# Kernel tuning notes

Hardware: AMD Instinct MI355X
Metric: run time of the kernel (lower is better)

## Reference

```python
import jax, jax.numpy as jnp
import numpy as np


def _rel_pos_log(ws):
    coords = np.stack(np.meshgrid(np.arange(ws), np.arange(ws), indexing='ij'))  # [2,ws,ws]
    cf = coords.reshape(2, -1)
    rel = (cf[:, :, None] - cf[:, None, :]).transpose(1, 2, 0).astype(np.float32)  # [N,N,2]
    return np.sign(rel) * np.log1p(np.abs(rel))


def _conv1x1(x, w, b):
    return jnp.einsum('bchw,oc->bohw', x, w) + b[None, :, None, None]


def _conv3x3_reflect(x, w, b):
    xp = jnp.pad(x, ((0, 0), (0, 0), (1, 1), (1, 1)), mode='reflect')
    y = jax.lax.conv_general_dilated(xp, w, (1, 1), 'VALID',
                                     dimension_numbers=('NCHW', 'OIHW', 'NCHW'))
    return y + b[None, :, None, None]


def setup_inputs() -> dict:
    key = jax.random.key(0)
    ks = jax.random.split(key, 8)
    dim, nh = 96, 6
    s = 0.02
    return {
        'X': jax.random.normal(ks[0], (4, dim, 256, 256), jnp.float32),
        'V_w': jax.random.normal(ks[1], (dim, dim), jnp.float32) * s,
        'V_b': jnp.zeros((dim,), jnp.float32),
        'QK_w': jax.random.normal(ks[2], (2 * dim, dim), jnp.float32) * s,
        'QK_b': jnp.zeros((2 * dim,), jnp.float32),
        'meta_w1': jax.random.normal(ks[3], (2, 256), jnp.float32) * 0.1,
        'meta_b1': jnp.zeros((256,), jnp.float32),
        'meta_w2': jax.random.normal(ks[4], (256, nh), jnp.float32) * 0.1,
        'meta_b2': jnp.zeros((nh,), jnp.float32),
        'conv1_w': jax.random.normal(ks[5], (dim, dim, 3, 3), jnp.float32) * s,
        'conv1_b': jnp.zeros((dim,), jnp.float32),
        'conv2_w': jax.random.normal(ks[6], (dim, dim, 3, 3), jnp.float32) * s,
        'conv2_b': jnp.zeros((dim,), jnp.float32),
        'proj_w': jax.random.normal(ks[7], (dim, dim), jnp.float32) * s,
        'proj_b': jnp.zeros((dim,), jnp.float32),
        'window_size': 8,
        'num_heads': 6,
    }


def reference(X, V_w, V_b, QK_w, QK_b, meta_w1, meta_b1, meta_w2, meta_b2,
              conv1_w, conv1_b, conv2_w, conv2_b, proj_w, proj_b,
              window_size, num_heads):
    B, C, H, W = X.shape
    ws = int(window_size)
    nh = int(num_heads)
    hd = C // nh
    scale = hd ** (-0.5)

    V = _conv1x1(X, V_w, V_b)                     # [B,C,H,W]
    QK = _conv1x1(X, QK_w, QK_b)                  # [B,2C,H,W]
    QKV = jnp.concatenate([QK, V], axis=1)        # [B,3C,H,W]

    # window partition (shift_size=0, H,W divisible by ws -> no padding)
    x = QKV.transpose(0, 2, 3, 1)                 # [B,H,W,3C]
    x = x.reshape(B, H // ws, ws, W // ws, ws, 3 * C)
    x = x.transpose(0, 1, 3, 2, 4, 5).reshape(-1, ws * ws, 3 * C)  # [nW,N,3C]

    qkv = x.reshape(-1, ws * ws, 3, nh, hd).transpose(2, 0, 3, 1, 4)
    q, k, v = qkv[0] * scale, qkv[1], qkv[2]      # [nW,nh,N,hd]
    attn = jnp.einsum('bhnd,bhmd->bhnm', q, k)    # [nW,nh,N,N]

    rp = jnp.asarray(_rel_pos_log(ws))            # [N,N,2]
    bias = jax.nn.relu(rp @ meta_w1 + meta_b1) @ meta_w2 + meta_b2  # [N,N,nh]
    attn = attn + bias.transpose(2, 0, 1)[None]
    attn = jax.nn.softmax(attn, axis=-1)

    o = jnp.einsum('bhnm,bhmd->bhnd', attn, v)    # [nW,nh,N,hd]
    o = o.transpose(0, 2, 1, 3).reshape(-1, ws * ws, C)

    # window reverse
    o = o.reshape(B, H // ws, W // ws, ws, ws, C)
    o = o.transpose(0, 1, 3, 2, 4, 5).reshape(B, H, W, C)
    attn_out = o.transpose(0, 3, 1, 2)            # [B,C,H,W]

    conv_out = _conv3x3_reflect(jax.nn.relu(_conv3x3_reflect(V, conv1_w, conv1_b)),
                                conv2_w, conv2_b)
    out = _conv1x1(conv_out + attn_out, proj_w, proj_b)
    return out
```

## Files before the change

### kernel.cpp

```cpp
#include <hip/hip_runtime.h>
#include <cmath>

typedef short  short8 __attribute__((ext_vector_type(8)));
typedef float  f32x4  __attribute__((ext_vector_type(4)));
typedef unsigned short us8 __attribute__((ext_vector_type(8)));
typedef unsigned short us4 __attribute__((ext_vector_type(4)));

constexpr int kHW = 65536;
constexpr int kP  = 262144;

__device__ __forceinline__ unsigned short f2bf(float x) {
  unsigned u = __builtin_bit_cast(unsigned, x);
  u += 0x7fffu + ((u >> 16) & 1u);
  return (unsigned short)(u >> 16);
}
__device__ __forceinline__ float bf2f(unsigned short h) {
  unsigned u = ((unsigned)h) << 16;
  return __builtin_bit_cast(float, u);
}
__device__ __forceinline__ void split2(float v, unsigned short& h, unsigned short& l) {
  unsigned short hh = f2bf(v);
  h = hh;
  l = f2bf(v - bf2f(hh));
}

__global__ void bias_kernel(const float* __restrict__ w1, const float* __restrict__ b1,
                            const float* __restrict__ w2, const float* __restrict__ b2,
                            float* __restrict__ bias_tab) {
  int i = blockIdx.x;
  int j = threadIdx.x;
  float dy = (float)((i >> 3) - (j >> 3));
  float dx = (float)((i & 7) - (j & 7));
  float r0 = copysignf(log1pf(fabsf(dy)), dy);
  float r1 = copysignf(log1pf(fabsf(dx)), dx);
  float acc[6];
#pragma unroll
  for (int h = 0; h < 6; ++h) acc[h] = b2[h];
  for (int t = 0; t < 256; ++t) {
    float hv = fmaf(r0, w1[t], fmaf(r1, w1[256 + t], b1[t]));
    hv = fmaxf(hv, 0.f);
#pragma unroll
    for (int h = 0; h < 6; ++h) acc[h] = fmaf(hv, w2[t * 6 + h], acc[h]);
  }
#pragma unroll
  for (int h = 0; h < 6; ++h) bias_tab[h * 4096 + i * 64 + j] = acc[h];
}

__global__ void prep_weights(const float* __restrict__ qk_w, const float* __restrict__ v_w,
                             const float* __restrict__ c1w, const float* __restrict__ c2w,
                             const float* __restrict__ pjw,
                             unsigned short* __restrict__ Wqh, unsigned short* __restrict__ Wql,
                             unsigned short* __restrict__ W1h,
                             unsigned short* __restrict__ W2h,
                             unsigned short* __restrict__ Wph, unsigned short* __restrict__ Wpl) {
  int i = blockIdx.x * 256 + threadIdx.x;
  if (i < 27648) {
    float v = (i < 18432) ? qk_w[i] : v_w[i - 18432];
    split2(v, Wqh[i], Wql[i]);
  }
  if (i < 82944) {
    int dlt = i / 9216;
    int oc  = (i / 96) % 96;
    int ic  = i % 96;
    int src = (oc * 96 + ic) * 9 + dlt;
    W1h[i] = f2bf(c1w[src]);
    W2h[i] = f2bf(c2w[src]);
  }
  if (i < 9216) split2(pjw[i], Wph[i], Wpl[i]);
}

__global__ __launch_bounds__(256) void split_x(const float* __restrict__ X,
                                               unsigned short* __restrict__ Xh) {
  __shared__ float tile[96][65];
  int t = threadIdx.x;
  size_t p0 = (size_t)blockIdx.x * 64;
  int b = (int)(p0 >> 16), pix = (int)(p0 & 65535);
  const float* xb = X + (size_t)b * 96 * kHW + pix;
#pragma unroll
  for (int i = 0; i < 24; ++i) {
    int ic = (t >> 6) + i * 4;
    tile[ic][t & 63] = xb[(size_t)ic * kHW + (t & 63)];
  }
  __syncthreads();
  int px = t >> 2;
  size_t outbase = (p0 + px) * 96;
#pragma unroll
  for (int cc = 0; cc < 3; ++cc) {
    int c = (t & 3) + cc * 4;
    us8 h8;
#pragma unroll
    for (int j = 0; j < 8; ++j) h8[j] = f2bf(tile[c * 8 + j][px]);
    *(us8*)(Xh + outbase + c * 8) = h8;
  }
}

__global__ __launch_bounds__(256, 2) void qkv_gemm(
    const unsigned short* __restrict__ Wqh, const unsigned short* __restrict__ Wql,
    const unsigned short* __restrict__ Xh,
    const float* __restrict__ qk_b, const float* __restrict__ v_b,
    unsigned short* __restrict__ Qp, unsigned short* __restrict__ Kp,
    unsigned short* __restrict__ Vp) {
  int t = threadIdx.x, wv = t >> 6, lane = t & 63;
  size_t px0 = (size_t)blockIdx.x * 256 + wv * 64;
  int col = lane & 15, g = lane >> 4;

  const char* bH = (const char*)Xh + ((px0 + col) * 96 + g * 8) * 2;
  short8 Bh[3][4];
#pragma unroll
  for (int ks = 0; ks < 3; ++ks)
#pragma unroll
    for (int nf = 0; nf < 4; ++nf)
      Bh[ks][nf] = *(const short8*)(bH + (size_t)(nf * 16 * 96 + ks * 32) * 2);

#pragma unroll 1
  for (int z = 0; z < 3; ++z) {
    f32x4 acc[6][4];
#pragma unroll
    for (int m = 0; m < 6; ++m)
#pragma unroll
      for (int n = 0; n < 4; ++n) acc[m][n] = (f32x4)0.f;
    const char* aH = (const char*)(Wqh + z * 9216) + (size_t)(col * 96 + g * 8) * 2;
    const char* aL = (const char*)(Wql + z * 9216) + (size_t)(col * 96 + g * 8) * 2;
#pragma unroll
    for (int ks = 0; ks < 3; ++ks) {
      short8 Ah[6], Al[6];
#pragma unroll
      for (int mf = 0; mf < 6; ++mf) {
        Ah[mf] = *(const short8*)(aH + (size_t)(mf * 16 * 96 + ks * 32) * 2);
        Al[mf] = *(const short8*)(aL + (size_t)(mf * 16 * 96 + ks * 32) * 2);
      }
#pragma unroll
      for (int mf = 0; mf < 6; ++mf)
#pragma unroll
        for (int nf = 0; nf < 4; ++nf) {
          acc[mf][nf] = __builtin_amdgcn_mfma_f32_16x16x32_bf16(Ah[mf], Bh[ks][nf], acc[mf][nf], 0, 0, 0);
          acc[mf][nf] = __builtin_amdgcn_mfma_f32_16x16x32_bf16(Al[mf], Bh[ks][nf], acc[mf][nf], 0, 0, 0);
        }
    }
    const float* bias = (z == 0) ? qk_b : (z == 1 ? qk_b + 96 : v_b);
    float scale = (z == 0) ? 0.25f : 1.f;
    unsigned short* dst = (z == 0) ? Qp : (z == 1 ? Kp : Vp);
#pragma unroll
    for (int mf = 0; mf < 6; ++mf) {
      int oc0 = mf * 16 + g * 4;
      int c8 = mf * 2 + (g >> 1);
      f32x4 bv;
#pragma unroll
      for (int r = 0; r < 4; ++r) bv[r] = bias[oc0 + r];
#pragma unroll
      for (int nf = 0; nf < 4; ++nf) {
        size_t p = px0 + nf * 16 + col;
        f32x4 v = (acc[mf][nf] + bv) * scale;
        us4 o;
#pragma unroll
        for (int r = 0; r < 4; ++r) o[r] = f2bf(v[r]);
        *(us4*)(dst + ((size_t)c8 * kP + p) * 8 + (g & 1) * 4) = o;
      }
    }
  }
}

__global__ __launch_bounds__(256) void attn_mfma(
    const unsigned short* __restrict__ Qp, const unsigned short* __restrict__ Kp,
    const unsigned short* __restrict__ Vp, const float* __restrict__ bias_tab,
    unsigned short* __restrict__ out) {
  __shared__ unsigned short PT[4][64 * 72];
  __shared__ unsigned short VT[4][16 * 72];
  __shared__ float rls[4][64];

  int t = threadIdx.x;
  int wv = t >> 6, lane = t & 63;
  int l15 = lane & 15, g = lane >> 4;
  int h = blockIdx.y;
  int wid = blockIdx.x * 4 + wv;
  int b = wid >> 10, wy = (wid >> 5) & 31, wx = wid & 31;
  size_t p0 = ((size_t)b << 16) + (size_t)wy * 8 * 256 + (size_t)wx * 8;
  const float* bt = bias_tab + h * 4096;

  f32x4 acc[4][4];
#pragma unroll
  for (int kf = 0; kf < 4; ++kf)
#pragma unroll
    for (int qf = 0; qf < 4; ++qf)
      acc[kf][qf] = *(const f32x4*)(bt + (qf * 16 + l15) * 64 + kf * 16 + g * 4);

  short8 Af[4], Bf[4];
#pragma unroll
  for (int f = 0; f < 4; ++f) {
    int kk = f * 16 + l15;
    size_t pk = p0 + (size_t)(kk >> 3) * 256 + (kk & 7);
    if (g < 2) {
      size_t pl = (size_t)(2 * h + g) * kP;
      Af[f] = *(const short8*)(Kp + (pl + pk) * 8);
      Bf[f] = *(const short8*)(Qp + (pl + pk) * 8);
    } else {
      Af[f] = (short8)0;
      Bf[f] = (short8)0;
    }
  }

  {
    size_t pv = p0 + (size_t)(lane >> 3) * 256 + (lane & 7);
    us8 v0 = *(const us8*)(Vp + ((size_t)(2 * h) * kP + pv) * 8);
    us8 v1 = *(const us8*)(Vp + ((size_t)(2 * h + 1) * kP + pv) * 8);
    unsigned short* vt = VT[wv];
#pragma unroll
    for (int d = 0; d < 8; ++d) {
      vt[d * 72 + lane]       = v0[d];
      vt[(d + 8) * 72 + lane] = v1[d];
    }
  }

#pragma unroll
  for (int kf = 0; kf < 4; ++kf)
#pragma unroll
    for (int qf = 0; qf < 4; ++qf)
      acc[kf][qf] = __builtin_amdgcn_mfma_f32_16x16x32_bf16(Af[kf], Bf[qf], acc[kf][qf], 0, 0, 0);

#pragma unroll
  for (int qf = 0; qf < 4; ++qf) {
    float m = acc[0][qf][0];
#pragma unroll
    for (int kf = 0; kf < 4; ++kf)
#pragma unroll
      for (int r = 0; r < 4; ++r) m = fmaxf(m, acc[kf][qf][r]);
    m = fmaxf(m, __shfl_xor(m, 16));
    m = fmaxf(m, __shfl_xor(m, 32));
    float sum = 0.f;
#pragma unroll
    for (int kf = 0; kf < 4; ++kf)
#pragma unroll
      for (int r = 0; r < 4; ++r) {
        float pe = __expf(acc[kf][qf][r] - m);
        acc[kf][qf][r] = pe;
        sum += pe;
      }
    sum += __shfl_xor(sum, 16);
    sum += __shfl_xor(sum, 32);
    if (g == 0) rls[wv][qf * 16 + l15] = 1.f / sum;
  }

  unsigned short* pt = PT[wv];
#pragma unroll
  for (int qf = 0; qf < 4; ++qf)
#pragma unroll
    for (int kf = 0; kf < 4; ++kf) {
      us4 pb;
#pragma unroll
      for (int r = 0; r < 4; ++r) pb[r] = f2bf(acc[kf][qf][r]);
      *(us4*)&pt[(qf * 16 + l15) * 72 + kf * 16 + g * 4] = pb;
    }

  short8 Pa[4][2], Vb[2];
#pragma unroll
  for (int qf = 0; qf < 4; ++qf)
#pragma unroll
    for (int kc = 0; kc < 2; ++kc)
      Pa[qf][kc] = *(const short8*)&pt[(qf * 16 + l15) * 72 + kc * 32 + g * 8];
#pragma unroll
  for (int kc = 0; kc < 2; ++kc)
    Vb[kc] = *(const short8*)&VT[wv][l15 * 72 + kc * 32 + g * 8];
  f32x4 o[4];
#pragma unroll
  for (int qf = 0; qf < 4; ++qf) {
    o[qf] = (f32x4)0.f;
#pragma unroll
    for (int kc = 0; kc < 2; ++kc)
      o[qf] = __builtin_amdgcn_mfma_f32_16x16x32_bf16(Pa[qf][kc], Vb[kc], o[qf], 0, 0, 0);
  }

#pragma unroll
  for (int qf = 0; qf < 4; ++qf) {
    f32x4 rv = *(const f32x4*)&rls[wv][qf * 16 + g * 4];
#pragma unroll
    for (int r = 0; r < 4; ++r)
      pt[(qf * 16 + g * 4 + r) * 72 + l15] = f2bf(o[qf][r] * rv[r]);
  }
  {
    int q = lane;
    us8 o0 = *(const us8*)&pt[q * 72];
    us8 o1 = *(const us8*)&pt[q * 72 + 8];
    size_t pq = p0 + (size_t)(q >> 3) * 256 + (q & 7);
    *(us8*)(out + ((size_t)(2 * h) * kP + pq) * 8)     = o0;
    *(us8*)(out + ((size_t)(2 * h + 1) * kP + pq) * 8) = o1;
  }
}

template <int MODE>
__global__ __launch_bounds__(256, 4) void conv_direct(
    const unsigned short* __restrict__ Wh,
    const unsigned short* __restrict__ B_, const float* __restrict__ bias,
    const unsigned short* __restrict__ attn, unsigned short* __restrict__ O_) {
  int t = threadIdx.x, wv = t >> 6, lane = t & 63;
  int col = lane & 15, g = lane >> 4;
  int och = wv >> 1, xq = wv & 1;
  int bid = blockIdx.x;
  int g8 = (bid & 7) * 256 + (bid >> 3);
  int xh = g8 & 1;
  int ry = g8 >> 1;
  int b = ry >> 8, y = ry & 255;
  int x0 = xh * 128 + xq * 64;

  int xc[4][3];
#pragma unroll
  for (int nf = 0; nf < 4; ++nf)
#pragma unroll
    for (int dx = 0; dx < 3; ++dx) {
      int xx = x0 + nf * 16 + col + dx - 1;
      xc[nf][dx] = xx < 0 ? 1 : (xx > 255 ? 254 : xx);
    }

  f32x4 acc[3][4];
#pragma unroll
  for (int m = 0; m < 3; ++m)
#pragma unroll
    for (int n = 0; n < 4; ++n) acc[m][n] = (f32x4)0.f;

  size_t bb = (size_t)b * kHW;
#pragma unroll
  for (int dy = 0; dy < 3; ++dy) {
    int yy = y + dy - 1;
    yy = yy < 0 ? 1 : (yy > 255 ? 254 : yy);
    size_t rowp = bb + (size_t)yy * 256;
#pragma unroll
    for (int dx = 0; dx < 3; ++dx) {
      const char* ah = (const char*)Wh +
          ((size_t)(dy * 3 + dx) * 9216 + och * 4608 + col * 96 + g * 8) * 2;
#pragma unroll
      for (int ks = 0; ks < 3; ++ks) {
        short8 Ah[3], Bf[4];
#pragma unroll
        for (int mf = 0; mf < 3; ++mf)
          Ah[mf] = *(const short8*)(ah + (size_t)(mf * 16 * 96 + ks * 32) * 2);
        size_t plane = (size_t)(ks * 4 + g) * kP;
#pragma unroll
        for (int nf = 0; nf < 4; ++nf)
          Bf[nf] = *(const short8*)(B_ + (plane + rowp + xc[nf][dx]) * 8);
#pragma unroll
        for (int mf = 0; mf < 3; ++mf)
#pragma unroll
          for (int nf = 0; nf < 4; ++nf)
            acc[mf][nf] = __builtin_amdgcn_mfma_f32_16x16x32_bf16(Ah[mf], Bf[nf], acc[mf][nf], 0, 0, 0);
      }
    }
  }

  size_t prow = bb + (size_t)y * 256;
#pragma unroll
  for (int mf = 0; mf < 3; ++mf) {
    int oc0 = och * 48 + mf * 16 + g * 4;
    int c8o = och * 6 + mf * 2 + (g >> 1);
    f32x4 bv;
#pragma unroll
    for (int r = 0; r < 4; ++r) bv[r] = bias[oc0 + r];
#pragma unroll
    for (int nf = 0; nf < 4; ++nf) {
      size_t p = prow + x0 + nf * 16 + col;
      f32x4 v = acc[mf][nf] + bv;
      if (MODE == 0) {
#pragma unroll
        for (int r = 0; r < 4; ++r) v[r] = fmaxf(v[r], 0.f);
      } else {
        us4 a4 = *(const us4*)(attn + ((size_t)c8o * kP + p) * 8 + (g & 1) * 4);
#pragma unroll
        for (int r = 0; r < 4; ++r) v[r] += bf2f(a4[r]);
      }
      us4 o;
#pragma unroll
      for (int r = 0; r < 4; ++r) o[r] = f2bf(v[r]);
      *(us4*)(O_ + ((size_t)c8o * kP + p) * 8 + (g & 1) * 4) = o;
    }
  }
}

__global__ __launch_bounds__(256, 2) void proj_gemm(
    const unsigned short* __restrict__ Wph, const unsigned short* __restrict__ Wpl,
    const unsigned short* __restrict__ S_, const float* __restrict__ bias,
    float* __restrict__ out) {
  int t = threadIdx.x, wv = t >> 6, lane = t & 63;
  size_t px0 = (size_t)blockIdx.x * 256 + wv * 64;
  int col = lane & 15, g = lane >> 4;
  f32x4 acc[6][4];
#pragma unroll
  for (int m = 0; m < 6; ++m)
#pragma unroll
    for (int n = 0; n < 4; ++n) acc[m][n] = (f32x4)0.f;
  const char* aH = (const char*)Wph + (size_t)(col * 96 + g * 8) * 2;
  const char* aL = (const char*)Wpl + (size_t)(col * 96 + g * 8) * 2;
#pragma unroll
  for (int ks = 0; ks < 3; ++ks) {
    short8 Ah[6], Al[6], Bf[4];
#pragma unroll
    for (int mf = 0; mf < 6; ++mf) {
      Ah[mf] = *(const short8*)(aH + (size_t)(mf * 16 * 96 + ks * 32) * 2);
      Al[mf] = *(const short8*)(aL + (size_t)(mf * 16 * 96 + ks * 32) * 2);
    }
    size_t plane = (size_t)(ks * 4 + g) * kP;
#pragma unroll
    for (int nf = 0; nf < 4; ++nf)
      Bf[nf] = *(const short8*)(S_ + (plane + px0 + nf * 16 + col) * 8);
#pragma unroll
    for (int mf = 0; mf < 6; ++mf)
#pragma unroll
      for (int nf = 0; nf < 4; ++nf) {
        acc[mf][nf] = __builtin_amdgcn_mfma_f32_16x16x32_bf16(Ah[mf], Bf[nf], acc[mf][nf], 0, 0, 0);
        acc[mf][nf] = __builtin_amdgcn_mfma_f32_16x16x32_bf16(Al[mf], Bf[nf], acc[mf][nf], 0, 0, 0);
      }
  }
#pragma unroll
  for (int mf = 0; mf < 6; ++mf) {
    int oc0 = mf * 16 + g * 4;
#pragma unroll
    for (int nf = 0; nf < 4; ++nf) {
      size_t p = px0 + nf * 16 + col;
      size_t bb = p >> 16, pix = p & 65535;
      f32x4 v = acc[mf][nf];
#pragma unroll
      for (int r = 0; r < 4; ++r)
        out[(bb * 96 + oc0 + r) * (size_t)kHW + pix] = v[r] + bias[oc0 + r];
    }
  }
}

extern "C" void kernel_launch(void* const* d_in, const int* in_sizes, int n_in,
                              void* d_out, int out_size, void* d_ws, size_t ws_size,
                              hipStream_t stream) {
  const float* X       = (const float*)d_in[0];
  const float* V_w     = (const float*)d_in[1];
  const float* V_b     = (const float*)d_in[2];
  const float* QK_w    = (const float*)d_in[3];
  const float* QK_b    = (const float*)d_in[4];
  const float* meta_w1 = (const float*)d_in[5];
  const float* meta_b1 = (const float*)d_in[6];
  const float* meta_w2 = (const float*)d_in[7];
  const float* meta_b2 = (const float*)d_in[8];
  const float* conv1_w = (const float*)d_in[9];
  const float* conv1_b = (const float*)d_in[10];
  const float* conv2_w = (const float*)d_in[11];
  const float* conv2_b = (const float*)d_in[12];
  const float* proj_w  = (const float*)d_in[13];
  const float* proj_b  = (const float*)d_in[14];
  float* out = (float*)d_out;

  char* w = (char*)d_ws;
  const size_t PLANE = (size_t)kP * 96 * 2;
  unsigned short* Xh = (unsigned short*)(w + 0 * PLANE);
  unsigned short* Qp = (unsigned short*)(w + 1 * PLANE);
  unsigned short* Kp = (unsigned short*)(w + 2 * PLANE);
  unsigned short* Vp = (unsigned short*)(w + 3 * PLANE);
  float* bias_tab    = (float*)(w + 4 * PLANE);
  unsigned short* Wqh = (unsigned short*)(w + 4 * PLANE + 98304);
  unsigned short* Wql = Wqh + 27648;
  unsigned short* W1h = Wql + 27648;
  unsigned short* W2h = W1h + 82944;
  unsigned short* Wph = W2h + 82944;
  unsigned short* Wpl = Wph + 9216;
  unsigned short* T1c = Xh;
  unsigned short* S2c = Qp;
  unsigned short* attnB = (unsigned short*)out;

  bias_kernel<<<dim3(64), dim3(64), 0, stream>>>(meta_w1, meta_b1, meta_w2, meta_b2, bias_tab);
  prep_weights<<<dim3(324), dim3(256), 0, stream>>>(QK_w, V_w, conv1_w, conv2_w, proj_w,
                                                    Wqh, Wql, W1h, W2h, Wph, Wpl);
  split_x<<<dim3(4096), dim3(256), 0, stream>>>(X, Xh);
  qkv_gemm<<<dim3(1024), dim3(256), 0, stream>>>(Wqh, Wql, Xh, QK_b, V_b, Qp, Kp, Vp);
  attn_mfma<<<dim3(1024, 6), dim3(256), 0, stream>>>(Qp, Kp, Vp, bias_tab, attnB);
  conv_direct<0><<<dim3(2048), dim3(256), 0, stream>>>(W1h, Vp, conv1_b, nullptr, T1c);
  conv_direct<1><<<dim3(2048), dim3(256), 0, stream>>>(W2h, T1c, conv2_b, attnB, S2c);
  proj_gemm<<<dim3(1024), dim3(256), 0, stream>>>(Wph, Wpl, S2c, proj_b, out);
}
```

Before: 390.0 us.

## Switch 3x3 convs to 32x32x16 MFMA with full-channel waves per row

Rewrites the direct 3x3 conv kernels to use 32x32x16 bf16 MFMA tiles. Each wave now computes all 96 output channels for 64 pixels, and each block covers a whole image row, so the grid is halved. Larger MFMA tiles mean fewer weight and activation fragment loads per FLOP and less redundant loading of B across channel halves. In exchange each thread holds more accumulator registers, which can lower occupancy, and the epilogue store pattern changes.

```diff
diff --git a/kernel.cpp b/kernel.cpp
--- a/kernel.cpp
+++ b/kernel.cpp
@@ -3,6 +3,7 @@
 
 typedef short  short8 __attribute__((ext_vector_type(8)));
 typedef float  f32x4  __attribute__((ext_vector_type(4)));
+typedef float  f32x16 __attribute__((ext_vector_type(16)));
 typedef unsigned short us8 __attribute__((ext_vector_type(8)));
 typedef unsigned short us4 __attribute__((ext_vector_type(4)));
 
@@ -287,34 +288,31 @@
 }
 
 template <int MODE>
-__global__ __launch_bounds__(256, 4) void conv_direct(
+__global__ __launch_bounds__(256, 4) void conv32(
     const unsigned short* __restrict__ Wh,
     const unsigned short* __restrict__ B_, const float* __restrict__ bias,
     const unsigned short* __restrict__ attn, unsigned short* __restrict__ O_) {
   int t = threadIdx.x, wv = t >> 6, lane = t & 63;
-  int col = lane & 15, g = lane >> 4;
-  int och = wv >> 1, xq = wv & 1;
+  int c31 = lane & 31, g2 = lane >> 5;
   int bid = blockIdx.x;
-  int g8 = (bid & 7) * 256 + (bid >> 3);
-  int xh = g8 & 1;
-  int ry = g8 >> 1;
-  int b = ry >> 8, y = ry & 255;
-  int x0 = xh * 128 + xq * 64;
-
-  int xc[4][3];
-#pragma unroll
-  for (int nf = 0; nf < 4; ++nf)
+  int g8 = (bid & 7) * 128 + (bid >> 3);
+  int b = g8 >> 8, y = g8 & 255;
+  int x0 = wv * 64;
+
+  int xc[2][3];
+#pragma unroll
+  for (int nf = 0; nf < 2; ++nf)
 #pragma unroll
     for (int dx = 0; dx < 3; ++dx) {
-      int xx = x0 + nf * 16 + col + dx - 1;
+      int xx = x0 + nf * 32 + c31 + dx - 1;
       xc[nf][dx] = xx < 0 ? 1 : (xx > 255 ? 254 : xx);
     }
 
-  f32x4 acc[3][4];
+  f32x16 acc[3][2];
 #pragma unroll
   for (int m = 0; m < 3; ++m)
 #pragma unroll
-    for (int n = 0; n < 4; ++n) acc[m][n] = (f32x4)0.f;
+    for (int n = 0; n < 2; ++n) acc[m][n] = (f32x16)0.f;
 
   size_t bb = (size_t)b * kHW;
 #pragma unroll
@@ -325,22 +323,22 @@
 #pragma unroll
     for (int dx = 0; dx < 3; ++dx) {
       const char* ah = (const char*)Wh +
-          ((size_t)(dy * 3 + dx) * 9216 + och * 4608 + col * 96 + g * 8) * 2;
-#pragma unroll
-      for (int ks = 0; ks < 3; ++ks) {
-        short8 Ah[3], Bf[4];
+          ((size_t)(dy * 3 + dx) * 9216 + c31 * 96 + g2 * 8) * 2;
+#pragma unroll
+      for (int ks = 0; ks < 6; ++ks) {
+        short8 Ah[3], Bf[2];
 #pragma unroll
         for (int mf = 0; mf < 3; ++mf)
-          Ah[mf] = *(const short8*)(ah + (size_t)(mf * 16 * 96 + ks * 32) * 2);
-        size_t plane = (size_t)(ks * 4 + g) * kP;
-#pragma unroll
-        for (int nf = 0; nf < 4; ++nf)
+          Ah[mf] = *(const short8*)(ah + (size_t)(mf * 32 * 96 + ks * 16) * 2);
+        size_t plane = (size_t)(ks * 2 + g2) * kP;
+#pragma unroll
+        for (int nf = 0; nf < 2; ++nf)
           Bf[nf] = *(const short8*)(B_ + (plane + rowp + xc[nf][dx]) * 8);
 #pragma unroll
         for (int mf = 0; mf < 3; ++mf)
 #pragma unroll
-          for (int nf = 0; nf < 4; ++nf)
-            acc[mf][nf] = __builtin_amdgcn_mfma_f32_16x16x32_bf16(Ah[mf], Bf[nf], acc[mf][nf], 0, 0, 0);
+          for (int nf = 0; nf < 2; ++nf)
+            acc[mf][nf] = __builtin_amdgcn_mfma_f32_32x32x16_bf16(Ah[mf], Bf[nf], acc[mf][nf], 0, 0, 0);
       }
     }
   }
@@ -348,27 +346,29 @@
   size_t prow = bb + (size_t)y * 256;
 #pragma unroll
   for (int mf = 0; mf < 3; ++mf) {
-    int oc0 = och * 48 + mf * 16 + g * 4;
-    int c8o = och * 6 + mf * 2 + (g >> 1);
-    f32x4 bv;
-#pragma unroll
-    for (int r = 0; r < 4; ++r) bv[r] = bias[oc0 + r];
-#pragma unroll
-    for (int nf = 0; nf < 4; ++nf) {
-      size_t p = prow + x0 + nf * 16 + col;
-      f32x4 v = acc[mf][nf] + bv;
-      if (MODE == 0) {
-#pragma unroll
-        for (int r = 0; r < 4; ++r) v[r] = fmaxf(v[r], 0.f);
-      } else {
-        us4 a4 = *(const us4*)(attn + ((size_t)c8o * kP + p) * 8 + (g & 1) * 4);
-#pragma unroll
-        for (int r = 0; r < 4; ++r) v[r] += bf2f(a4[r]);
-      }
-      us4 o;
-#pragma unroll
-      for (int r = 0; r < 4; ++r) o[r] = f2bf(v[r]);
-      *(us4*)(O_ + ((size_t)c8o * kP + p) * 8 + (g & 1) * 4) = o;
+#pragma unroll
+    for (int nf = 0; nf < 2; ++nf) {
+      size_t p = prow + x0 + nf * 32 + c31;
+#pragma unroll
+      for (int q = 0; q < 4; ++q) {
+        int oc0 = mf * 32 + q * 8 + g2 * 4;
+        int c8o = mf * 4 + q;
+        f32x4 v;
+#pragma unroll
+        for (int r = 0; r < 4; ++r) v[r] = acc[mf][nf][q * 4 + r] + bias[oc0 + r];
+        if (MODE == 0) {
+#pragma unroll
+          for (int r = 0; r < 4; ++r) v[r] = fmaxf(v[r], 0.f);
+        } else {
+          us4 a4 = *(const us4*)(attn + ((size_t)c8o * kP + p) * 8 + g2 * 4);
+#pragma unroll
+          for (int r = 0; r < 4; ++r) v[r] += bf2f(a4[r]);
+        }
+        us4 o;
+#pragma unroll
+        for (int r = 0; r < 4; ++r) o[r] = f2bf(v[r]);
+        *(us4*)(O_ + ((size_t)c8o * kP + p) * 8 + g2 * 4) = o;
+      }
     }
   }
 }
@@ -465,7 +465,7 @@
   split_x<<<dim3(4096), dim3(256), 0, stream>>>(X, Xh);
   qkv_gemm<<<dim3(1024), dim3(256), 0, stream>>>(Wqh, Wql, Xh, QK_b, V_b, Qp, Kp, Vp);
   attn_mfma<<<dim3(1024, 6), dim3(256), 0, stream>>>(Qp, Kp, Vp, bias_tab, attnB);
-  conv_direct<0><<<dim3(2048), dim3(256), 0, stream>>>(W1h, Vp, conv1_b, nullptr, T1c);
-  conv_direct<1><<<dim3(2048), dim3(256), 0, stream>>>(W2h, T1c, conv2_b, attnB, S2c);
+  conv32<0><<<dim3(1024), dim3(256), 0, stream>>>(W1h, Vp, conv1_b, nullptr, T1c);
+  conv32<1><<<dim3(1024), dim3(256), 0, stream>>>(W2h, T1c, conv2_b, attnB, S2c);
   proj_gemm<<<dim3(1024), dim3(256), 0, stream>>>(Wph, Wpl, S2c, proj_b, out);
 }
```

After: 1.129 ms. +189.5%, slower.
